# Kernel optimization log

Hardware: AMD Instinct MI355X
Metric: run time of the kernel (lower is better)

The kernel has to match this reference:

```python
import jax, jax.numpy as jnp
import numpy as np

B, S = 8, 1024
DM = 512            # d_model arg
D = 2 * DM          # actual feature width (1024)
H = 16
DK = D // H         # 64
DV = 2 * 32         # per-head value dim (2*d_v) = 64
DI = 2048           # d_inner
K = 4               # d_conv, dilation 2 -> effective 7, pad 3 each side
EPS = 1e-6


def setup_inputs() -> dict:
    key = jax.random.key(0)
    ks = jax.random.split(key, 16)
    s = lambda k, shape, fan: jax.random.normal(k, shape, jnp.float32) / np.sqrt(fan)
    return {
        "x": jax.random.normal(ks[0], (B, S, D), jnp.float32),
        "mask": jnp.ones((B, 1, 1, S), jnp.int32),
        "gamma": jnp.ones((D,), jnp.float32),
        "wq": s(ks[1], (D, H * DK), D),
        "wk": s(ks[2], (D, H * DK), D),
        "wv": s(ks[3], (D, H * DV), D),
        "wo": s(ks[4], (H * DV, D), H * DV),
        "w1": s(ks[5], (DM, DI), DM),
        "b1": jnp.zeros((DI,), jnp.float32),
        "cw": s(ks[6], (DI, 1, K), K),   # depthwise conv kernel [O, I/groups=1, K]
        "cb": jnp.zeros((DI,), jnp.float32),
        "w2": s(ks[7], (DM, DI), DM),
        "b2": jnp.zeros((DI,), jnp.float32),
        "wp": s(ks[8], (DI, D), DI),
        "bp": jnp.zeros((D,), jnp.float32),
    }


def reference(x, mask, gamma, wq, wk, wv, wo, w1, b1, cw, cb, w2, b2, wp, bp):
    # RMSNorm
    nrm = x * jax.lax.rsqrt(jnp.mean(x * x, axis=-1, keepdims=True) + EPS) * gamma
    # Multi-head attention
    q = (nrm @ wq).reshape(B, S, H, DK).transpose(0, 2, 1, 3)
    k = (nrm @ wk).reshape(B, S, H, DK).transpose(0, 2, 1, 3)
    v = (nrm @ wv).reshape(B, S, H, DV).transpose(0, 2, 1, 3)
    scores = jnp.einsum('bhqd,bhkd->bhqk', q, k) / np.sqrt(DK).astype(np.float32)
    scores = jnp.where(mask == 0, jnp.float32(-1e9), scores)
    attn = jax.nn.softmax(scores, axis=-1)
    ctx = jnp.einsum('bhqk,bhkd->bhqd', attn, v)        # [B,H,S,DV]
    ctx = ctx.transpose(0, 2, 1, 3).reshape(B, S, H * DV)
    out = ctx @ wo                                       # [B,S,D]
    # split into two halves
    f_in, s_in = out[:, :, :D // 2], out[:, :, D // 2:]
    # FirstSection: linear -> depthwise dilated conv (padding 'same')
    f = f_in @ w1 + b1                                   # [B,S,DI]
    f = f.transpose(0, 2, 1)                             # [B,DI,S]
    f = jax.lax.conv_general_dilated(
        f, cw, window_strides=(1,), padding=[(3, 3)], rhs_dilation=(2,),
        feature_group_count=DI, dimension_numbers=('NCH', 'OIH', 'NCH'))
    f = (f + cb[None, :, None]).transpose(0, 2, 1)       # [B,S,DI]
    # SecondSection: linear + relu
    sec = jax.nn.relu(s_in @ w2 + b2)                    # [B,S,DI]
    gated = f * sec
    return x + (gated @ wp + bp)
```

## Files before the change

kernel.cpp:

```cpp
#include <hip/hip_runtime.h>

typedef unsigned short u16;
typedef __bf16 bf16x8 __attribute__((ext_vector_type(8)));
typedef short  s16x8  __attribute__((ext_vector_type(8)));
typedef float  f32x4  __attribute__((ext_vector_type(4)));

#define LDSPAD 72

#define GLOAD16(gp, lp) __builtin_amdgcn_global_load_lds( \
  (__attribute__((address_space(1))) unsigned int*)(unsigned long long)(const void*)(gp), \
  (__attribute__((address_space(3))) unsigned int*)(lp), 16, 0, 0)

static __device__ __forceinline__ u16 f2bf(float f){
  union { float f; unsigned int u; } v; v.f = f;
  unsigned int r = v.u + 0x7fffu + ((v.u >> 16) & 1u);
  return (u16)(r >> 16);
}
static __device__ __forceinline__ float bf2f(u16 u){
  union { unsigned int u; float f; } v; v.u = ((unsigned int)u) << 16; return v.f;
}
static __device__ __forceinline__ unsigned fbits(float f){
  union { float f; unsigned u; } v; v.f = f; return v.u;
}

__global__ __launch_bounds__(256) void wtrans_kernel(const float* __restrict__ in,
                                                     u16* __restrict__ out, int K, int N){
  __shared__ float tile[32][33];
  int n0 = blockIdx.x * 32, k0 = blockIdx.y * 32;
  int tx = threadIdx.x, ty = threadIdx.y;
  #pragma unroll
  for (int i = 0; i < 4; ++i)
    tile[ty + i*8][tx] = in[(size_t)(k0 + ty + i*8) * N + n0 + tx];
  __syncthreads();
  #pragma unroll
  for (int i = 0; i < 4; ++i)
    out[(size_t)(n0 + ty + i*8) * K + k0 + tx] = f2bf(tile[tx][ty + i*8]);
}

__global__ __launch_bounds__(256) void cwtrans_kernel(const float* __restrict__ cw,
                                                      float* __restrict__ cwT){
  int i = blockIdx.x * 256 + threadIdx.x;
  int c = i >> 2, j = i & 3;
  cwT[j * 2048 + c] = cw[i];
}

__global__ __launch_bounds__(256) void rmsnorm_kernel(const float* __restrict__ x,
                                                      const float* __restrict__ gamma,
                                                      u16* __restrict__ out){
  int row = blockIdx.x;
  const float* xr = x + (size_t)row * 1024;
  int tid = threadIdx.x;
  float4 xv = *(const float4*)(xr + tid * 4);
  float ss = xv.x*xv.x + xv.y*xv.y + xv.z*xv.z + xv.w*xv.w;
  #pragma unroll
  for (int off = 1; off < 64; off <<= 1) ss += __shfl_xor(ss, off);
  __shared__ float wsum[4];
  if ((tid & 63) == 0) wsum[tid >> 6] = ss;
  __syncthreads();
  float tot = wsum[0] + wsum[1] + wsum[2] + wsum[3];
  float r = rsqrtf(tot * (1.0f/1024.0f) + 1e-6f);
  const float4 gv = *(const float4*)(gamma + tid * 4);
  u16* o = out + (size_t)row * 1024 + tid * 4;
  o[0] = f2bf(xv.x * r * gv.x);
  o[1] = f2bf(xv.y * r * gv.y);
  o[2] = f2bf(xv.z * r * gv.z);
  o[3] = f2bf(xv.w * r * gv.w);
}

template<int EPI>
__global__ __launch_bounds__(256) void gemm128_kernel(
    const u16* __restrict__ A, int lda,
    const u16* __restrict__ Bt,
    const float* __restrict__ bias,
    const float* __restrict__ resid,
    u16* __restrict__ outb, float* __restrict__ outf,
    u16* __restrict__ vt,
    int N, int K, float scale, int nm)
{
  __shared__ __align__(16) u16 As[2][128*64];
  __shared__ __align__(16) u16 Bs[2][128*64];
  int tid = threadIdx.x;
  int wid = tid >> 6, lane = tid & 63;
  int fr = lane & 15, fq = lane >> 4;
  int wr = wid >> 1, wc = wid & 1;
  int l = ((int)blockIdx.x & 7) * ((int)gridDim.x >> 3) + ((int)blockIdx.x >> 3);
  int m0 = (l % nm) * 128, n0 = (l / nm) * 128;
  int srow = lane >> 3;
  int csw  = (lane & 7) ^ srow;
  int c7   = fr & 7;
  f32x4 acc[4][4] = {};

  const u16* Abase = A  + (size_t)m0 * lda;
  const u16* Bbase = Bt + (size_t)n0 * K;

  auto STAGE = [&](int bsel, int kt){
    int k0 = kt << 6;
    #pragma unroll
    for (int i = 0; i < 4; ++i){
      int r = i*32 + wid*8;
      GLOAD16(Abase + (size_t)(r + srow) * lda + k0 + csw*8, &As[bsel][r*64]);
      GLOAD16(Bbase + (size_t)(r + srow) * K   + k0 + csw*8, &Bs[bsel][r*64]);
    }
  };

  int nt = K >> 6;
  STAGE(0, 0);
  __syncthreads();
  for (int kt = 0; kt < nt; ++kt){
    int cur = kt & 1;
    if (kt + 1 < nt) STAGE(cur ^ 1, kt + 1);
    #pragma unroll
    for (int ks = 0; ks < 2; ++ks){
      bf16x8 av[4], bv[4];
      #pragma unroll
      for (int mi = 0; mi < 4; ++mi)
        av[mi] = *(const bf16x8*)&As[cur][(wr*64 + mi*16 + fr)*64 + (((ks*4 + fq) ^ c7) * 8)];
      #pragma unroll
      for (int ni = 0; ni < 4; ++ni)
        bv[ni] = *(const bf16x8*)&Bs[cur][(wc*64 + ni*16 + fr)*64 + (((ks*4 + fq) ^ c7) * 8)];
      #pragma unroll
      for (int mi = 0; mi < 4; ++mi)
        #pragma unroll
        for (int ni = 0; ni < 4; ++ni)
          acc[mi][ni] = __builtin_amdgcn_mfma_f32_16x16x32_bf16(av[mi], bv[ni], acc[mi][ni], 0, 0, 0);
    }
    __syncthreads();
  }

  if (EPI == 5 && n0 >= 2048){
    u16* Ct = &As[0][0];
    #pragma unroll
    for (int p = 0; p < 2; ++p){
      __syncthreads();
      if (wc == p){
        #pragma unroll
        for (int ni = 0; ni < 4; ++ni)
          #pragma unroll
          for (int mi = 0; mi < 4; ++mi){
            int cl = ni*16 + fr;
            int rl = wr*64 + mi*16 + fq*4;
            uint2 pk;
            pk.x = (unsigned)f2bf(acc[mi][ni][0]) | ((unsigned)f2bf(acc[mi][ni][1]) << 16);
            pk.y = (unsigned)f2bf(acc[mi][ni][2]) | ((unsigned)f2bf(acc[mi][ni][3]) << 16);
            *(uint2*)&Ct[cl*136 + rl] = pk;
          }
      }
      __syncthreads();
      #pragma unroll
      for (int ci = 0; ci < 4; ++ci){
        int qq = ci*256 + tid;
        int c = qq >> 4, off = (qq & 15) * 8;
        uint4 v = *(const uint4*)&Ct[c*136 + off];
        *(uint4*)&vt[(size_t)(n0 - 2048 + p*64 + c) * 8192 + m0 + off] = v;
      }
    }
    return;
  }

  #pragma unroll
  for (int ni = 0; ni < 4; ++ni){
    int col = n0 + wc*64 + ni*16 + fr;
    float bvv = (EPI >= 1 && EPI <= 3) ? bias[col] : 0.0f;
    float scl = (EPI == 5) ? ((col < 1024) ? scale : 1.0f) : scale;
    #pragma unroll
    for (int mi = 0; mi < 4; ++mi){
      #pragma unroll
      for (int j = 0; j < 4; ++j){
        int row = m0 + wr*64 + mi*16 + fq*4 + j;
        float vv = acc[mi][ni][j] * scl + bvv;
        if (EPI == 2) vv = fmaxf(vv, 0.0f);
        size_t idx = (size_t)row * N + col;
        if (EPI == 3) outf[idx] = vv + resid[idx];
        else          outb[idx] = f2bf(vv);
      }
    }
  }
}

__global__ __launch_bounds__(256) void attn_kernel(
    const u16* __restrict__ qkv, const u16* __restrict__ Vt,
    const int* __restrict__ mask, u16* __restrict__ ctx)
{
  __shared__ __align__(16) u16 Ks[64*64];
  __shared__ __align__(16) u16 Vs[64*64];
  __shared__ __align__(16) u16 Ps[64][LDSPAD];
  int tid = threadIdx.x;
  int wid = tid >> 6, lane = tid & 63;
  int fr = lane & 15, fq = lane >> 4;
  int q0 = blockIdx.x * 64;
  int bh = blockIdx.y;
  int b = bh >> 4, h = bh & 15;

  const u16* qb  = qkv + (size_t)b * 1024 * 3072 + h * 64;
  const u16* kb  = qb + 1024;
  const u16* vtb = Vt + (size_t)(h * 64) * 8192 + b * 1024;

  int lrow = lane >> 3;
  int cs   = (lane & 7) ^ lrow;
  int wbase = wid * 16;

  bf16x8 qf[2];
  {
    const u16* qp = qb + (size_t)(q0 + wid*16 + fr) * 3072 + fq * 8;
    qf[0] = *(const bf16x8*)(qp);
    qf[1] = *(const bf16x8*)(qp + 32);
  }
  f32x4 acc[4];
  #pragma unroll
  for (int i = 0; i < 4; ++i) acc[i] = (f32x4){0.f, 0.f, 0.f, 0.f};
  float m = -1e30f, lsum = 0.f;
  int c7 = fr & 7;

  for (int t = 0; t < 16; ++t){
    int kv0 = t * 64;
    __syncthreads();
    #pragma unroll
    for (int i = 0; i < 2; ++i){
      int r = wbase + i*8 + lrow;
      GLOAD16(kb  + (size_t)(kv0 + r) * 3072 + cs * 8, &Ks[(wbase + i*8) * 64]);
      GLOAD16(vtb + (size_t)r * 8192 + kv0 + cs * 8,   &Vs[(wbase + i*8) * 64]);
    }
    __syncthreads();

    f32x4 sc[4];
    #pragma unroll
    for (int nt = 0; nt < 4; ++nt) sc[nt] = (f32x4){0.f, 0.f, 0.f, 0.f};
    __builtin_amdgcn_s_setprio(1);
    #pragma unroll
    for (int ks = 0; ks < 2; ++ks){
      #pragma unroll
      for (int nt = 0; nt < 4; ++nt){
        bf16x8 kv = *(const bf16x8*)&Ks[(nt*16 + fr)*64 + (((ks*4 + fq) ^ c7) * 8)];
        sc[nt] = __builtin_amdgcn_mfma_f32_16x16x32_bf16(kv, qf[ks], sc[nt], 0, 0, 0);
      }
    }
    __builtin_amdgcn_s_setprio(0);

    #pragma unroll
    for (int nt = 0; nt < 4; ++nt){
      int4 mv = *(const int4*)&mask[b * 1024 + kv0 + nt*16 + fq*4];
      int mvals[4] = {mv.x, mv.y, mv.z, mv.w};
      #pragma unroll
      for (int j = 0; j < 4; ++j)
        sc[nt][j] = mvals[j] ? sc[nt][j] : -1e9f;
    }

    float pmax = -1e30f;
    #pragma unroll
    for (int nt = 0; nt < 4; ++nt)
      #pragma unroll
      for (int j = 0; j < 4; ++j)
        pmax = fmaxf(pmax, sc[nt][j]);
    pmax = fmaxf(pmax, __shfl_xor(pmax, 16));
    pmax = fmaxf(pmax, __shfl_xor(pmax, 32));
    if (!__all(pmax <= m + 8.0f)){
      float mnew = fmaxf(m, pmax);
      float corr = exp2f(m - mnew);
      #pragma unroll
      for (int nt = 0; nt < 4; ++nt)
        #pragma unroll
        for (int j = 0; j < 4; ++j)
          acc[nt][j] *= corr;
      lsum *= corr;
      m = mnew;
    }
    float p[4][4];
    float ls = 0.f;
    #pragma unroll
    for (int nt = 0; nt < 4; ++nt)
      #pragma unroll
      for (int j = 0; j < 4; ++j){
        float pv = exp2f(sc[nt][j] - m);
        p[nt][j] = pv;
        ls += pv;
      }
    lsum += ls;

    #pragma unroll
    for (int nt = 0; nt < 4; ++nt){
      unsigned d0 = __builtin_amdgcn_perm(fbits(p[nt][1]), fbits(p[nt][0]), 0x07060302u);
      unsigned d1 = __builtin_amdgcn_perm(fbits(p[nt][3]), fbits(p[nt][2]), 0x07060302u);
      *(unsigned*)&Ps[wid*16 + fr][nt*16 + fq*4]     = d0;
      *(unsigned*)&Ps[wid*16 + fr][nt*16 + fq*4 + 2] = d1;
    }

    __builtin_amdgcn_s_setprio(1);
    #pragma unroll
    for (int ks = 0; ks < 2; ++ks){
      bf16x8 pb = *(const bf16x8*)&Ps[wid*16 + fr][ks*32 + fq*8];
      #pragma unroll
      for (int nt = 0; nt < 4; ++nt){
        bf16x8 vv = *(const bf16x8*)&Vs[(nt*16 + fr)*64 + (((ks*4 + fq) ^ c7) * 8)];
        acc[nt] = __builtin_amdgcn_mfma_f32_16x16x32_bf16(vv, pb, acc[nt], 0, 0, 0);
      }
    }
    __builtin_amdgcn_s_setprio(0);
  }

  lsum += __shfl_xor(lsum, 16);
  lsum += __shfl_xor(lsum, 32);
  float invl = 1.0f / lsum;

  size_t rowbase = ((size_t)b * 1024 + q0 + wid*16 + fr) * 1024 + h * 64;
  #pragma unroll
  for (int nt = 0; nt < 4; ++nt){
    unsigned lo = (unsigned)f2bf(acc[nt][0] * invl) | ((unsigned)f2bf(acc[nt][1] * invl) << 16);
    unsigned hi = (unsigned)f2bf(acc[nt][2] * invl) | ((unsigned)f2bf(acc[nt][3] * invl) << 16);
    uint2 pk; pk.x = lo; pk.y = hi;
    *(uint2*)&ctx[rowbase + nt*16 + fq*4] = pk;
  }
}

__global__ __launch_bounds__(256) void convgate_kernel(
    const u16* __restrict__ f, const float* __restrict__ cwT,
    const float* __restrict__ cb, u16* __restrict__ sec_inout)
{
  size_t gid = (size_t)blockIdx.x * blockDim.x + threadIdx.x;
  int c0 = (int)(gid & 255) * 8;
  int t  = (int)((gid >> 8) & 1023);
  int b  = (int)(gid >> 18);
  const u16* fb = f + ((size_t)b * 1024) * 2048;

  float4 w[4][2];
  #pragma unroll
  for (int j = 0; j < 4; ++j){
    w[j][0] = *(const float4*)&cwT[j*2048 + c0];
    w[j][1] = *(const float4*)&cwT[j*2048 + c0 + 4];
  }
  float4 cb0 = *(const float4*)&cb[c0];
  float4 cb1 = *(const float4*)&cb[c0 + 4];
  float acc[8] = {cb0.x, cb0.y, cb0.z, cb0.w, cb1.x, cb1.y, cb1.z, cb1.w};

  #pragma unroll
  for (int j = 0; j < 4; ++j){
    int tt = t - 3 + 2 * j;
    if (tt >= 0 && tt < 1024){
      s16x8 fv = *(const s16x8*)(fb + (size_t)tt * 2048 + c0);
      const float* wj = (const float*)&w[j][0];
      #pragma unroll
      for (int e = 0; e < 8; ++e) acc[e] += bf2f((u16)fv[e]) * wj[e];
    }
  }
  u16* sp = sec_inout + (((size_t)b * 1024 + t) * 2048 + c0);
  s16x8 sv = *(const s16x8*)sp;
  s16x8 ov;
  #pragma unroll
  for (int e = 0; e < 8; ++e) ov[e] = (short)f2bf(acc[e] * bf2f((u16)sv[e]));
  *(s16x8*)sp = ov;
}

extern "C" void kernel_launch(void* const* d_in, const int* in_sizes, int n_in,
                              void* d_out, int out_size, void* d_ws, size_t ws_size,
                              hipStream_t stream)
{
  const float* x     = (const float*)d_in[0];
  const int*   mask  = (const int*)  d_in[1];
  const float* gamma = (const float*)d_in[2];
  const float* wq    = (const float*)d_in[3];
  const float* wk    = (const float*)d_in[4];
  const float* wv    = (const float*)d_in[5];
  const float* wo    = (const float*)d_in[6];
  const float* w1    = (const float*)d_in[7];
  const float* b1    = (const float*)d_in[8];
  const float* cw    = (const float*)d_in[9];
  const float* cb    = (const float*)d_in[10];
  const float* w2    = (const float*)d_in[11];
  const float* b2    = (const float*)d_in[12];
  const float* wp    = (const float*)d_in[13];
  const float* bp    = (const float*)d_in[14];
  float* out = (float*)d_out;

  char* p = (char*)d_ws;
  auto alloc = [&](size_t bytes){ char* r = p; p += (bytes + 255) & ~(size_t)255; return r; };
  u16*   wqkvT = (u16*)alloc((size_t)3072*1024*2);
  u16*   woT   = (u16*)alloc((size_t)1024*1024*2);
  u16*   w1T   = (u16*)alloc((size_t)2048*512*2);
  u16*   w2T   = (u16*)alloc((size_t)2048*512*2);
  u16*   wpT   = (u16*)alloc((size_t)1024*2048*2);
  float* cwT   = (float*)alloc((size_t)4*2048*4);
  u16*   nrm   = (u16*)alloc((size_t)8192*1024*2);
  u16*   qkv   = (u16*)alloc((size_t)8192*3072*2);
  u16*   sec   = (u16*)alloc((size_t)8192*2048*2);
  u16* Vt   = sec;
  u16* ao   = qkv;
  u16* fbuf = qkv + (size_t)8192*1024;
  (void)ws_size; (void)in_sizes; (void)n_in; (void)out_size;

  const float QSCALE = 0.125f * 1.44269504088896340736f;

  dim3 tb32(32, 8);
  wtrans_kernel<<<dim3(32, 32), tb32, 0, stream>>>(wq, wqkvT,                     1024, 1024);
  wtrans_kernel<<<dim3(32, 32), tb32, 0, stream>>>(wk, wqkvT + (size_t)1024*1024, 1024, 1024);
  wtrans_kernel<<<dim3(32, 32), tb32, 0, stream>>>(wv, wqkvT + (size_t)2048*1024, 1024, 1024);
  wtrans_kernel<<<dim3(32, 32), tb32, 0, stream>>>(wo, woT, 1024, 1024);
  wtrans_kernel<<<dim3(64, 16), tb32, 0, stream>>>(w1, w1T, 512, 2048);
  wtrans_kernel<<<dim3(64, 16), tb32, 0, stream>>>(w2, w2T, 512, 2048);
  wtrans_kernel<<<dim3(32, 64), tb32, 0, stream>>>(wp, wpT, 2048, 1024);
  cwtrans_kernel<<<32, 256, 0, stream>>>(cw, cwT);

  rmsnorm_kernel<<<8192, 256, 0, stream>>>(x, gamma, nrm);

  gemm128_kernel<5><<<1536, 256, 0, stream>>>(nrm, 1024, wqkvT, nullptr, nullptr, qkv, nullptr, Vt, 3072, 1024, QSCALE, 64);

  attn_kernel<<<dim3(16, 128), 256, 0, stream>>>(qkv, Vt, mask, nrm);

  gemm128_kernel<0><<<512, 256, 0, stream>>>(nrm, 1024, woT, nullptr, nullptr, ao, nullptr, nullptr, 1024, 1024, 1.0f, 64);

  gemm128_kernel<1><<<1024, 256, 0, stream>>>(ao,       1024, w1T, b1, nullptr, fbuf, nullptr, nullptr, 2048, 512, 1.0f, 64);
  gemm128_kernel<2><<<1024, 256, 0, stream>>>(ao + 512, 1024, w2T, b2, nullptr, sec,  nullptr, nullptr, 2048, 512, 1.0f, 64);

  convgate_kernel<<<8192, 256, 0, stream>>>(fbuf, cwT, cb, sec);

  gemm128_kernel<3><<<512, 256, 0, stream>>>(sec, 2048, wpT, bp, x, nullptr, out, nullptr, 1024, 2048, 1.0f, 64);
}
```

Baseline: 354.6 us.

## Prefetch next KV tile in attention, batch weight transposes, remap block indices

The attention kernel now copies each K/V tile from LDS into registers and then issues the global-to-LDS load for the next tile, so the loads overlap with the MFMA and softmax work. Mask application is skipped when every mask value in the tile is nonzero. The max reduction becomes a tree. Attention workgroups are remapped onto a 1D grid with an interleave of stride 8, apparently to spread related blocks across XCDs. The GEMM drops its XCD-swizzled block mapping in favour of linear order, and the seven weight-transpose launches are merged into three multi-slice launches. The register-held K/V fragments raise VGPR pressure, and the GEMM remap may hurt L2 locality.

After: 311.9 us. 12.1% less time.

```diff
diff --git a/kernel.cpp b/kernel.cpp
--- a/kernel.cpp
+++ b/kernel.cpp
@@ -23,9 +23,15 @@
   union { float f; unsigned u; } v; v.f = f; return v.u;
 }
 
-__global__ __launch_bounds__(256) void wtrans_kernel(const float* __restrict__ in,
-                                                     u16* __restrict__ out, int K, int N){
+__global__ __launch_bounds__(256) void wtrans4_kernel(
+    const float* __restrict__ in0, const float* __restrict__ in1,
+    const float* __restrict__ in2, const float* __restrict__ in3,
+    u16* __restrict__ out0, u16* __restrict__ out1,
+    u16* __restrict__ out2, u16* __restrict__ out3, int K, int N){
   __shared__ float tile[32][33];
+  int z = blockIdx.z;
+  const float* in = (z == 0) ? in0 : (z == 1) ? in1 : (z == 2) ? in2 : in3;
+  u16* out = (z == 0) ? out0 : (z == 1) ? out1 : (z == 2) ? out2 : out3;
   int n0 = blockIdx.x * 32, k0 = blockIdx.y * 32;
   int tx = threadIdx.x, ty = threadIdx.y;
   #pragma unroll
@@ -83,7 +89,7 @@
   int wid = tid >> 6, lane = tid & 63;
   int fr = lane & 15, fq = lane >> 4;
   int wr = wid >> 1, wc = wid & 1;
-  int l = ((int)blockIdx.x & 7) * ((int)gridDim.x >> 3) + ((int)blockIdx.x >> 3);
+  int l = (int)blockIdx.x;
   int m0 = (l % nm) * 128, n0 = (l / nm) * 128;
   int srow = lane >> 3;
   int csw  = (lane & 7) ^ srow;
@@ -187,8 +193,10 @@
   int tid = threadIdx.x;
   int wid = tid >> 6, lane = tid & 63;
   int fr = lane & 15, fq = lane >> 4;
-  int q0 = blockIdx.x * 64;
-  int bh = blockIdx.y;
+  int i = (int)blockIdx.x;
+  int wg = (i & 7) * 256 + (i >> 3);
+  int bh = wg >> 4;
+  int q0 = (wg & 15) * 64;
   int b = bh >> 4, h = bh & 15;
 
   const u16* qb  = qkv + (size_t)b * 1024 * 3072 + h * 64;
@@ -198,6 +206,7 @@
   int lrow = lane >> 3;
   int cs   = (lane & 7) ^ lrow;
   int wbase = wid * 16;
+  int c7 = fr & 7;
 
   bf16x8 qf[2];
   {
@@ -207,62 +216,74 @@
   }
   f32x4 acc[4];
   #pragma unroll
-  for (int i = 0; i < 4; ++i) acc[i] = (f32x4){0.f, 0.f, 0.f, 0.f};
-  float m = -1e30f, lsum = 0.f;
-  int c7 = fr & 7;
-
+  for (int k = 0; k < 4; ++k) acc[k] = (f32x4){0.f, 0.f, 0.f, 0.f};
+  float mrun = -1e30f, lsum = 0.f;
+
+  auto STAGE = [&](int t){
+    int kv0 = t * 64;
+    #pragma unroll
+    for (int k = 0; k < 2; ++k){
+      int r = wbase + k*8 + lrow;
+      GLOAD16(kb  + (size_t)(kv0 + r) * 3072 + cs * 8, &Ks[(wbase + k*8) * 64]);
+      GLOAD16(vtb + (size_t)r * 8192 + kv0 + cs * 8,   &Vs[(wbase + k*8) * 64]);
+    }
+  };
+
+  STAGE(0);
   for (int t = 0; t < 16; ++t){
     int kv0 = t * 64;
     __syncthreads();
-    #pragma unroll
-    for (int i = 0; i < 2; ++i){
-      int r = wbase + i*8 + lrow;
-      GLOAD16(kb  + (size_t)(kv0 + r) * 3072 + cs * 8, &Ks[(wbase + i*8) * 64]);
-      GLOAD16(vtb + (size_t)r * 8192 + kv0 + cs * 8,   &Vs[(wbase + i*8) * 64]);
-    }
+    bf16x8 kf[2][4], vf[2][4];
+    #pragma unroll
+    for (int ks = 0; ks < 2; ++ks)
+      #pragma unroll
+      for (int nt = 0; nt < 4; ++nt){
+        kf[ks][nt] = *(const bf16x8*)&Ks[(nt*16 + fr)*64 + (((ks*4 + fq) ^ c7) * 8)];
+        vf[ks][nt] = *(const bf16x8*)&Vs[(nt*16 + fr)*64 + (((ks*4 + fq) ^ c7) * 8)];
+      }
+    int mv1 = mask[b * 1024 + kv0 + lane];
     __syncthreads();
+    if (t + 1 < 16) STAGE(t + 1);
 
     f32x4 sc[4];
     #pragma unroll
     for (int nt = 0; nt < 4; ++nt) sc[nt] = (f32x4){0.f, 0.f, 0.f, 0.f};
     __builtin_amdgcn_s_setprio(1);
     #pragma unroll
-    for (int ks = 0; ks < 2; ++ks){
+    for (int ks = 0; ks < 2; ++ks)
+      #pragma unroll
+      for (int nt = 0; nt < 4; ++nt)
+        sc[nt] = __builtin_amdgcn_mfma_f32_16x16x32_bf16(kf[ks][nt], qf[ks], sc[nt], 0, 0, 0);
+    __builtin_amdgcn_s_setprio(0);
+
+    if (!__all(mv1 != 0)){
       #pragma unroll
       for (int nt = 0; nt < 4; ++nt){
-        bf16x8 kv = *(const bf16x8*)&Ks[(nt*16 + fr)*64 + (((ks*4 + fq) ^ c7) * 8)];
-        sc[nt] = __builtin_amdgcn_mfma_f32_16x16x32_bf16(kv, qf[ks], sc[nt], 0, 0, 0);
-      }
-    }
-    __builtin_amdgcn_s_setprio(0);
-
-    #pragma unroll
-    for (int nt = 0; nt < 4; ++nt){
-      int4 mv = *(const int4*)&mask[b * 1024 + kv0 + nt*16 + fq*4];
-      int mvals[4] = {mv.x, mv.y, mv.z, mv.w};
-      #pragma unroll
-      for (int j = 0; j < 4; ++j)
-        sc[nt][j] = mvals[j] ? sc[nt][j] : -1e9f;
-    }
-
-    float pmax = -1e30f;
-    #pragma unroll
-    for (int nt = 0; nt < 4; ++nt)
-      #pragma unroll
-      for (int j = 0; j < 4; ++j)
-        pmax = fmaxf(pmax, sc[nt][j]);
+        int4 mv = *(const int4*)&mask[b * 1024 + kv0 + nt*16 + fq*4];
+        int mvals[4] = {mv.x, mv.y, mv.z, mv.w};
+        #pragma unroll
+        for (int j = 0; j < 4; ++j)
+          sc[nt][j] = mvals[j] ? sc[nt][j] : -1e9f;
+      }
+    }
+
+    float m01 = fmaxf(fmaxf(sc[0][0], sc[0][1]), fmaxf(sc[0][2], sc[0][3]));
+    float m11 = fmaxf(fmaxf(sc[1][0], sc[1][1]), fmaxf(sc[1][2], sc[1][3]));
+    float m21 = fmaxf(fmaxf(sc[2][0], sc[2][1]), fmaxf(sc[2][2], sc[2][3]));
+    float m31 = fmaxf(fmaxf(sc[3][0], sc[3][1]), fmaxf(sc[3][2], sc[3][3]));
+    float pmax = fmaxf(fmaxf(m01, m11), fmaxf(m21, m31));
     pmax = fmaxf(pmax, __shfl_xor(pmax, 16));
     pmax = fmaxf(pmax, __shfl_xor(pmax, 32));
-    if (!__all(pmax <= m + 8.0f)){
-      float mnew = fmaxf(m, pmax);
-      float corr = exp2f(m - mnew);
+    if (!__all(pmax <= mrun + 8.0f)){
+      float mnew = fmaxf(mrun, pmax);
+      float corr = exp2f(mrun - mnew);
       #pragma unroll
       for (int nt = 0; nt < 4; ++nt)
         #pragma unroll
         for (int j = 0; j < 4; ++j)
           acc[nt][j] *= corr;
       lsum *= corr;
-      m = mnew;
+      mrun = mnew;
     }
     float p[4][4];
     float ls = 0.f;
@@ -270,7 +291,7 @@
     for (int nt = 0; nt < 4; ++nt)
       #pragma unroll
       for (int j = 0; j < 4; ++j){
-        float pv = exp2f(sc[nt][j] - m);
+        float pv = exp2f(sc[nt][j] - mrun);
         p[nt][j] = pv;
         ls += pv;
       }
@@ -289,10 +310,8 @@
     for (int ks = 0; ks < 2; ++ks){
       bf16x8 pb = *(const bf16x8*)&Ps[wid*16 + fr][ks*32 + fq*8];
       #pragma unroll
-      for (int nt = 0; nt < 4; ++nt){
-        bf16x8 vv = *(const bf16x8*)&Vs[(nt*16 + fr)*64 + (((ks*4 + fq) ^ c7) * 8)];
-        acc[nt] = __builtin_amdgcn_mfma_f32_16x16x32_bf16(vv, pb, acc[nt], 0, 0, 0);
-      }
+      for (int nt = 0; nt < 4; ++nt)
+        acc[nt] = __builtin_amdgcn_mfma_f32_16x16x32_bf16(vf[ks][nt], pb, acc[nt], 0, 0, 0);
     }
     __builtin_amdgcn_s_setprio(0);
   }
@@ -389,20 +408,20 @@
   const float QSCALE = 0.125f * 1.44269504088896340736f;
 
   dim3 tb32(32, 8);
-  wtrans_kernel<<<dim3(32, 32), tb32, 0, stream>>>(wq, wqkvT,                     1024, 1024);
-  wtrans_kernel<<<dim3(32, 32), tb32, 0, stream>>>(wk, wqkvT + (size_t)1024*1024, 1024, 1024);
-  wtrans_kernel<<<dim3(32, 32), tb32, 0, stream>>>(wv, wqkvT + (size_t)2048*1024, 1024, 1024);
-  wtrans_kernel<<<dim3(32, 32), tb32, 0, stream>>>(wo, woT, 1024, 1024);
-  wtrans_kernel<<<dim3(64, 16), tb32, 0, stream>>>(w1, w1T, 512, 2048);
-  wtrans_kernel<<<dim3(64, 16), tb32, 0, stream>>>(w2, w2T, 512, 2048);
-  wtrans_kernel<<<dim3(32, 64), tb32, 0, stream>>>(wp, wpT, 2048, 1024);
+  wtrans4_kernel<<<dim3(32, 32, 4), tb32, 0, stream>>>(
+      wq, wk, wv, wo,
+      wqkvT, wqkvT + (size_t)1024*1024, wqkvT + (size_t)2048*1024, woT, 1024, 1024);
+  wtrans4_kernel<<<dim3(64, 16, 2), tb32, 0, stream>>>(
+      w1, w2, w1, w2, w1T, w2T, w1T, w2T, 512, 2048);
+  wtrans4_kernel<<<dim3(32, 64, 1), tb32, 0, stream>>>(
+      wp, wp, wp, wp, wpT, wpT, wpT, wpT, 2048, 1024);
   cwtrans_kernel<<<32, 256, 0, stream>>>(cw, cwT);
 
   rmsnorm_kernel<<<8192, 256, 0, stream>>>(x, gamma, nrm);
 
   gemm128_kernel<5><<<1536, 256, 0, stream>>>(nrm, 1024, wqkvT, nullptr, nullptr, qkv, nullptr, Vt, 3072, 1024, QSCALE, 64);
 
-  attn_kernel<<<dim3(16, 128), 256, 0, stream>>>(qkv, Vt, mask, nrm);
+  attn_kernel<<<2048, 256, 0, stream>>>(qkv, Vt, mask, nrm);
 
   gemm128_kernel<0><<<512, 256, 0, stream>>>(nrm, 1024, woT, nullptr, nullptr, ao, nullptr, nullptr, 1024, 1024, 1.0f, 64);
 
```
